# Kernel optimization log

Hardware: AMD Instinct MI355X
Metric: run time of the kernel (lower is better)

The kernel has to match this reference:

```python
import jax, jax.numpy as jnp
import numpy as np

EPS = 1e-12
TEMPERATURE = 0.1
QUEUE_SIZE = 1024
CUTOFF_KM = 25.0
EARTH_R_KM = 6371.0088


def _normalize(x, axis=-1):
    n = jnp.linalg.norm(x, axis=axis, keepdims=True)
    return x / jnp.maximum(n, EPS)


def _haversine_km(a, b):
    # a: (B,1,2), b: (1,S,2) in degrees (lat, lon) -> (B,S) km
    ra, rb = jnp.deg2rad(a), jnp.deg2rad(b)
    dlat = rb[..., 0] - ra[..., 0]
    dlon = rb[..., 1] - ra[..., 1]
    h = jnp.sin(dlat / 2) ** 2 + jnp.cos(ra[..., 0]) * jnp.cos(rb[..., 0]) * jnp.sin(dlon / 2) ** 2
    return 2.0 * EARTH_R_KM * jnp.arcsin(jnp.sqrt(jnp.clip(h, 0.0, 1.0)))


def setup_inputs() -> dict:
    key = jax.random.key(0)
    k1, k2, k3, k4, k5 = jax.random.split(key, 5)
    A, B, F, S = 3, 256, 512, 100000
    V = jax.random.normal(k1, (A, B, F), dtype=jnp.float32)
    L = jax.random.normal(k2, (B, F), dtype=jnp.float32)
    # gps as (lat, lon) degrees
    gps = jax.random.uniform(k3, (B, 2), dtype=jnp.float32) * jnp.array([120.0, 360.0]) - jnp.array([60.0, 180.0])
    support_feats = jax.random.normal(k4, (S, F), dtype=jnp.float32)
    support_gps = jax.random.uniform(k5, (S, 2), dtype=jnp.float32) * jnp.array([120.0, 360.0]) - jnp.array([60.0, 180.0])
    return {"V": V, "L": L, "gps": gps, "support_feats": support_feats, "support_gps": support_gps}


def reference(V, L, gps, support_feats, support_gps):
    T, Q = TEMPERATURE, QUEUE_SIZE
    L_norm = _normalize(L, axis=1)                      # (B,F)
    org = _normalize(V[0] * L_norm, axis=1)             # (B,F)
    aug = _normalize(V[1:] * L_norm, axis=2)            # (A-1,B,F)

    # nearest_neighbours (no_grad): per-batch NN in support set by dot-product sim
    sims = jnp.einsum('sf,bf->sb', support_feats, org)  # (S,B)
    nn_idx = jnp.argmax(sims, axis=0)                   # (B,)
    nn = _normalize(support_feats[nn_idx], axis=1)      # (B,F)
    nn = jax.lax.stop_gradient(nn)

    pos = jnp.exp(jnp.einsum('abf,bf->ab', aug, nn) / T)  # (A-1,B)
    batch_den = jnp.sum(pos, axis=0)                       # (B,)

    # nn_negative_queue (no_grad): first Q support rows farther than 25 km, zeros if fewer
    dist = _haversine_km(gps[:, None, :], support_gps[None, :, :])  # (B,S)
    far = dist > CUTOFF_KM                                          # (B,S)
    order = jnp.argsort(jnp.logical_not(far), axis=1)[:, :Q]        # stable: far rows first, in order
    valid = jnp.take_along_axis(far, order, axis=1)                 # (B,Q)
    negq = jnp.where(valid[..., None], support_feats[order], 0.0)   # (B,Q,F)
    negq = jax.lax.stop_gradient(_normalize(negq, axis=2))          # zero rows stay zero

    queue_den = jnp.sum(jnp.exp(jnp.einsum('bqf,bf->bq', negq, nn) / T), axis=1)  # (B,)

    loss = jnp.mean(-batch_den / (batch_den + queue_den))
    return loss
```

## Files before the change

kernel.cpp:

```cpp
#include <hip/hip_runtime.h>
#include <hip/hip_bf16.h>
#include <math.h>

#define B_N 256
#define F_N 512
#define S_N 100000
#define Q_N 1024
#define EPSF 1e-12f
#define BM 128
#define NBLK ((S_N + BM - 1) / BM)

typedef __attribute__((ext_vector_type(8))) short short8v;
typedef __attribute__((ext_vector_type(4))) float f32x4;

__device__ __forceinline__ unsigned short f2bf(float x) {
  unsigned u = __float_as_uint(x);
  u = u + 0x7FFFu + ((u >> 16) & 1u);
  return (unsigned short)(u >> 16);
}
__device__ __forceinline__ float bf2f(unsigned short h) {
  return __uint_as_float(((unsigned)h) << 16);
}

__device__ __forceinline__ float warpReduceSum(float v) {
  #pragma unroll
  for (int o = 32; o > 0; o >>= 1) v += __shfl_down(v, o);
  return v;
}

__device__ __forceinline__ float blockReduceSum256(float v, float* buf) {
  v = warpReduceSum(v);
  int lane = threadIdx.x & 63, w = threadIdx.x >> 6;
  __syncthreads();
  if (lane == 0) buf[w] = v;
  __syncthreads();
  return buf[0] + buf[1] + buf[2] + buf[3];
}

__device__ __forceinline__ void async_copy16(void* lds, const void* g) {
  __builtin_amdgcn_global_load_lds(
      (const __attribute__((address_space(1))) unsigned int*)g,
      (__attribute__((address_space(3))) unsigned int*)lds, 16, 0, 0);
}

__device__ __forceinline__ void cvt8(const float4 a, const float4 b,
                                     short8v& hi, short8v& lo) {
  union { unsigned u[4]; short8v v; } H, L;
  float xs[8] = {a.x, a.y, a.z, a.w, b.x, b.y, b.z, b.w};
  #pragma unroll
  for (int i = 0; i < 4; ++i) {
    float p = xs[2 * i], q = xs[2 * i + 1];
    union { __hip_bfloat162 b2; unsigned u; } c;
    c.b2 = __float22bfloat162_rn(make_float2(p, q));
    H.u[i] = c.u;
    float rp = p - __uint_as_float(c.u << 16);
    float rq = q - __uint_as_float(c.u & 0xFFFF0000u);
    union { __hip_bfloat162 b2; unsigned u; } d;
    d.b2 = __float22bfloat162_rn(make_float2(rp, rq));
    L.u[i] = d.u;
  }
  hi = H.v; lo = L.v;
}

__global__ __launch_bounds__(256) void k_prep(const float* __restrict__ V,
    const float* __restrict__ L, unsigned short* __restrict__ orgst,
    float* __restrict__ aug, unsigned long long* __restrict__ keys) {
  __shared__ float buf[4];
  int b = blockIdx.x, t = threadIdx.x;
  if (t == 0) keys[b] = 0ull;
  const float2 lv = *(const float2*)&L[b * F_N + t * 2];
  float ss = blockReduceSum256(lv.x * lv.x + lv.y * lv.y, buf);
  float invL = 1.0f / fmaxf(sqrtf(ss), EPSF);
  float lnx = lv.x * invL, lny = lv.y * invL;
  #pragma unroll
  for (int a = 0; a < 3; ++a) {
    const float2 vv = *(const float2*)&V[(a * B_N + b) * F_N + t * 2];
    float yx = vv.x * lnx, yy = vv.y * lny;
    float s2 = blockReduceSum256(yx * yx + yy * yy, buf);
    float inv = 1.0f / fmaxf(sqrtf(s2), EPSF);
    if (a == 0) {
      float ox = yx * inv, oy = yy * inv;
      int f = t * 2;
      int kt = f >> 5, kk = f & 31, sub = kk >> 3, pos = kk & 7;
      unsigned short hx = f2bf(ox), hy = f2bf(oy);
      unsigned short lx = f2bf(ox - bf2f(hx)), ly = f2bf(oy - bf2f(hy));
      int base = kt * 16384 + b * 64;
      ushort2 hv; hv.x = hx; hv.y = hy;
      ushort2 lw; lw.x = lx; lw.y = ly;
      *(ushort2*)&orgst[base + ((sub ^ (b & 7)) << 3) + pos] = hv;
      *(ushort2*)&orgst[base + (((sub | 4) ^ (b & 7)) << 3) + pos] = lw;
    } else {
      float* dst = &aug[((a - 1) * B_N + b) * F_N + t * 2];
      dst[0] = yx * inv;
      dst[1] = yy * inv;
    }
  }
}

__global__ __launch_bounds__(256, 3) void k_sims(const float* __restrict__ support,
    const unsigned short* __restrict__ orgst, unsigned long long* __restrict__ keys) {
  __shared__ __align__(16) unsigned char smem[32768];

  int t = threadIdx.x;
  int lane = t & 63, w = t >> 6;
  int r15 = lane & 15, ks = lane >> 4;
  int bid = blockIdx.x;
  int half = (bid >= NBLK) ? 1 : 0;
  int s0 = (half ? bid - NBLK : bid) * BM;

  f32x4 acc0[8], acc1[8];
  #pragma unroll
  for (int n = 0; n < 8; ++n) {
    acc0[n] = (f32x4){0.f, 0.f, 0.f, 0.f};
    acc1[n] = (f32x4){0.f, 0.f, 0.f, 0.f};
  }

  int row0 = s0 + w * 32 + r15;
  int row1 = row0 + 16;
  if (row0 > S_N - 1) row0 = S_N - 1;
  if (row1 > S_N - 1) row1 = S_N - 1;
  const float* ap0 = support + (size_t)row0 * F_N + ks * 8;
  const float* ap1 = support + (size_t)row1 * F_N + ks * 8;

  const unsigned char* bsrc =
      (const unsigned char*)orgst + half * 16384 + t * 16;

  {
    unsigned char* dst = smem + t * 16;
    #pragma unroll
    for (int p = 0; p < 4; ++p) async_copy16(dst + p * 4096, bsrc + p * 4096);
  }
  float4 a0a = *(const float4*)(ap0);
  float4 a0b = *(const float4*)(ap0 + 4);
  float4 a1a = *(const float4*)(ap1);
  float4 a1b = *(const float4*)(ap1 + 4);
  short8v fh0, fl0, fh1, fl1;
  cvt8(a0a, a0b, fh0, fl0);
  cvt8(a1a, a1b, fh1, fl1);
  __syncthreads();

  const int hioff = (ks ^ (r15 & 7)) << 4;
  const int looff = ((ks | 4) ^ (r15 & 7)) << 4;

  #pragma unroll 1
  for (int kt = 0; kt < 16; ++kt) {
    unsigned char* bbuf = smem + (kt & 1) * 16384;
    if (kt < 15) {
      a0a = *(const float4*)(ap0 + (kt + 1) * 32);
      a0b = *(const float4*)(ap0 + (kt + 1) * 32 + 4);
      a1a = *(const float4*)(ap1 + (kt + 1) * 32);
      a1b = *(const float4*)(ap1 + (kt + 1) * 32 + 4);
      __builtin_amdgcn_sched_barrier(0);
      const unsigned char* src = bsrc + (kt + 1) * 32768;
      unsigned char* dst = smem + ((kt + 1) & 1) * 16384 + t * 16;
      #pragma unroll
      for (int p = 0; p < 4; ++p) async_copy16(dst + p * 4096, src + p * 4096);
      __builtin_amdgcn_sched_barrier(0);
    }
    const unsigned char* bp = bbuf + r15 * 128 + hioff;
    const unsigned char* bq = bbuf + r15 * 128 + looff;
    __builtin_amdgcn_s_setprio(1);
    #pragma unroll
    for (int n = 0; n < 8; ++n) {
      short8v bh = *(const short8v*)(bp + n * 2048);
      short8v bl = *(const short8v*)(bq + n * 2048);
      acc0[n] = __builtin_amdgcn_mfma_f32_16x16x32_bf16(fh0, bh, acc0[n], 0, 0, 0);
      acc1[n] = __builtin_amdgcn_mfma_f32_16x16x32_bf16(fh1, bh, acc1[n], 0, 0, 0);
      acc0[n] = __builtin_amdgcn_mfma_f32_16x16x32_bf16(fl0, bh, acc0[n], 0, 0, 0);
      acc1[n] = __builtin_amdgcn_mfma_f32_16x16x32_bf16(fl1, bh, acc1[n], 0, 0, 0);
      acc0[n] = __builtin_amdgcn_mfma_f32_16x16x32_bf16(fh0, bl, acc0[n], 0, 0, 0);
      acc1[n] = __builtin_amdgcn_mfma_f32_16x16x32_bf16(fh1, bl, acc1[n], 0, 0, 0);
    }
    __builtin_amdgcn_s_setprio(0);
    __builtin_amdgcn_sched_barrier(0);
    if (kt < 15) {
      cvt8(a0a, a0b, fh0, fl0);
      cvt8(a1a, a1b, fh1, fl1);
      __builtin_amdgcn_sched_barrier(0);
      asm volatile("s_waitcnt vmcnt(0)" ::: "memory");
      __builtin_amdgcn_s_barrier();
      __builtin_amdgcn_sched_barrier(0);
    } else {
      __syncthreads();
    }
  }

  unsigned long long* wk = (unsigned long long*)smem;
  #pragma unroll
  for (int n = 0; n < 8; ++n) {
    float bv = -INFINITY;
    int bi = 0x7FFFFFFF;
    #pragma unroll
    for (int r = 0; r < 4; ++r) {
      int sA = s0 + w * 32 + ks * 4 + r;
      float vA = acc0[n][r];
      if (sA < S_N && (vA > bv || (vA == bv && sA < bi))) { bv = vA; bi = sA; }
      int sB = sA + 16;
      float vB = acc1[n][r];
      if (sB < S_N && (vB > bv || (vB == bv && sB < bi))) { bv = vB; bi = sB; }
    }
    #pragma unroll
    for (int mask = 16; mask <= 32; mask <<= 1) {
      float ov = __shfl_xor(bv, mask);
      int oi = __shfl_xor(bi, mask);
      if (ov > bv || (ov == bv && oi < bi)) { bv = ov; bi = oi; }
    }
    if (lane < 16) {
      unsigned u = __float_as_uint(bv);
      u = (u & 0x80000000u) ? ~u : (u | 0x80000000u);
      wk[w * 128 + n * 16 + lane] =
          ((unsigned long long)u << 32) |
          (unsigned long long)(0xFFFFFFFFu - (unsigned)bi);
    }
  }
  __syncthreads();
  if (t < 128) {
    unsigned long long k0 = wk[t], k1 = wk[128 + t];
    unsigned long long k2 = wk[256 + t], k3 = wk[384 + t];
    unsigned long long m01 = k0 > k1 ? k0 : k1;
    unsigned long long m23 = k2 > k3 ? k2 : k3;
    atomicMax(&keys[half * 128 + t], m01 > m23 ? m01 : m23);
  }
}

__global__ __launch_bounds__(256) void k_nn(const float* __restrict__ support,
    const unsigned long long* __restrict__ keys, const float* __restrict__ aug,
    float* __restrict__ nn, float* __restrict__ bden) {
  __shared__ float buf[4];
  int b = blockIdx.x, t = threadIdx.x;
  int idx = (int)(0xFFFFFFFFu - (unsigned)(keys[b] & 0xFFFFFFFFull));
  const float2 rv = *(const float2*)&support[(size_t)idx * F_N + t * 2];
  float ss = blockReduceSum256(rv.x * rv.x + rv.y * rv.y, buf);
  float inv = 1.0f / fmaxf(sqrtf(ss), EPSF);
  float nx = rv.x * inv, ny = rv.y * inv;
  nn[b * F_N + t * 2] = nx;
  nn[b * F_N + t * 2 + 1] = ny;
  const float2 a0 = *(const float2*)&aug[(0 * B_N + b) * F_N + t * 2];
  const float2 a1 = *(const float2*)&aug[(1 * B_N + b) * F_N + t * 2];
  float d0 = blockReduceSum256(a0.x * nx + a0.y * ny, buf);
  float d1 = blockReduceSum256(a1.x * nx + a1.y * ny, buf);
  if (t == 0) bden[b] = expf(d0 * 10.0f) + expf(d1 * 10.0f);
}

__global__ __launch_bounds__(256) void k_qdot(const float* __restrict__ support,
    const float* __restrict__ gps, const float* __restrict__ sgps,
    const float* __restrict__ nn, double* __restrict__ qpart) {
  __shared__ float nns[F_N];
  __shared__ int qi[256];
  __shared__ int wtot[4];
  __shared__ double wacc[4];
  int b = blockIdx.x >> 2, c = blockIdx.x & 3;
  int t = threadIdx.x;
  int lane = t & 63, w = t >> 6;

  *(float2*)&nns[t * 2] = *(const float2*)&nn[b * F_N + t * 2];

  const float DEG2RAD = 0.017453292519943295f;
  float la = gps[b * 2] * DEG2RAD;
  float lo = gps[b * 2 + 1] * DEG2RAD;
  float ca = cosf(la);
  double xd = 25.0 / (2.0 * 6371.0088);
  float hcut = (float)(sin(xd) * sin(xd));

  int cnt = 0;
  int qlo = c * 256;
  for (int base = 0; base < S_N; base += 256) {
    int s = base + t;
    bool far = false;
    if (s < S_N) {
      float lb = sgps[s * 2] * DEG2RAD;
      float ob = sgps[s * 2 + 1] * DEG2RAD;
      float sl = sinf((lb - la) * 0.5f);
      float so = sinf((ob - lo) * 0.5f);
      float h = sl * sl + ca * cosf(lb) * so * so;
      far = h > hcut;
    }
    unsigned long long m = __ballot(far);
    if (lane == 0) wtot[w] = (int)__popcll(m);
    __syncthreads();
    int offs = cnt;
    for (int wi = 0; wi < w; ++wi) offs += wtot[wi];
    if (far) {
      int pos = offs + (int)__popcll(m & ((1ull << lane) - 1ull));
      int rel = pos - qlo;
      if (rel >= 0 && rel < 256) qi[rel] = s;
    }
    cnt += wtot[0] + wtot[1] + wtot[2] + wtot[3];
    __syncthreads();
    if (cnt >= Q_N) break;
  }
  int nvalid = cnt < Q_N ? cnt : Q_N;
  __syncthreads();

  double acc = 0.0;
  for (int j = 0; j < 64; ++j) {
    int q = qlo + w * 64 + j;
    if (q >= nvalid) break;
    int row = qi[w * 64 + j];
    const float4* rp = (const float4*)&support[(size_t)row * F_N + lane * 8];
    float4 r0 = rp[0], r1 = rp[1];
    const float4 n0 = *(const float4*)&nns[lane * 8];
    const float4 n1 = *(const float4*)&nns[lane * 8 + 4];
    float dot = r0.x * n0.x + r0.y * n0.y + r0.z * n0.z + r0.w * n0.w +
                r1.x * n1.x + r1.y * n1.y + r1.z * n1.z + r1.w * n1.w;
    float ssq = r0.x * r0.x + r0.y * r0.y + r0.z * r0.z + r0.w * r0.w +
                r1.x * r1.x + r1.y * r1.y + r1.z * r1.z + r1.w * r1.w;
    #pragma unroll
    for (int o = 32; o > 0; o >>= 1) {
      dot += __shfl_xor(dot, o);
      ssq += __shfl_xor(ssq, o);
    }
    float val = dot / fmaxf(sqrtf(ssq), EPSF);
    acc += (double)expf(val * 10.0f);
  }
  if (lane == 0) wacc[w] = acc;
  __syncthreads();
  if (t == 0) {
    int got = nvalid - qlo;
    if (got < 0) got = 0; if (got > 256) got = 256;
    int inval = 256 - got;
    qpart[blockIdx.x] = wacc[0] + wacc[1] + wacc[2] + wacc[3] + (double)inval;
  }
}

__global__ __launch_bounds__(256) void k_final(const double* __restrict__ qpart,
    const float* __restrict__ bden, float* __restrict__ out) {
  __shared__ double buf[4];
  int t = threadIdx.x;
  double qd = qpart[t * 4] + qpart[t * 4 + 1] + qpart[t * 4 + 2] + qpart[t * 4 + 3];
  double bd = (double)bden[t];
  double v = -bd / (bd + qd);
  #pragma unroll
  for (int o = 32; o > 0; o >>= 1) v += __shfl_down(v, o);
  if ((t & 63) == 0) buf[t >> 6] = v;
  __syncthreads();
  if (t == 0) out[0] = (float)((buf[0] + buf[1] + buf[2] + buf[3]) / 256.0);
}

extern "C" void kernel_launch(void* const* d_in, const int* in_sizes, int n_in,
                              void* d_out, int out_size, void* d_ws, size_t ws_size,
                              hipStream_t stream) {
  const float* V = (const float*)d_in[0];
  const float* L = (const float*)d_in[1];
  const float* gps = (const float*)d_in[2];
  const float* support = (const float*)d_in[3];
  const float* sgps = (const float*)d_in[4];
  float* out = (float*)d_out;

  char* ws = (char*)d_ws;
  unsigned long long* keys = (unsigned long long*)ws;
  float* bden = (float*)(ws + 2048);
  double* qpart = (double*)(ws + 4096);
  unsigned short* orgst = (unsigned short*)(ws + 12288);
  float* aug = (float*)(ws + 12288 + 524288);
  float* nn = (float*)(ws + 12288 + 524288 + 1048576);

  k_prep<<<256, 256, 0, stream>>>(V, L, orgst, aug, keys);
  k_sims<<<2 * NBLK, 256, 0, stream>>>(support, orgst, keys);
  k_nn<<<256, 256, 0, stream>>>(support, keys, aug, nn, bden);
  k_qdot<<<1024, 256, 0, stream>>>(support, gps, sgps, nn, qpart);
  k_final<<<1, 256, 0, stream>>>(qpart, bden, out);
}
```

Before: 190.6 us.

## Use single-bf16 sims with per-block maxima, then exact FP64 rescoring of candidates

Result: no change. 191.8 us (+0.6%).

```diff
diff --git a/kernel.cpp b/kernel.cpp
--- a/kernel.cpp
+++ b/kernel.cpp
@@ -9,6 +9,8 @@
 #define EPSF 1e-12f
 #define BM 128
 #define NBLK ((S_N + BM - 1) / BM)
+#define CAND_MAX 64
+#define MARGIN 0.125f
 
 typedef __attribute__((ext_vector_type(8))) short short8v;
 typedef __attribute__((ext_vector_type(4))) float f32x4;
@@ -18,9 +20,6 @@
   u = u + 0x7FFFu + ((u >> 16) & 1u);
   return (unsigned short)(u >> 16);
 }
-__device__ __forceinline__ float bf2f(unsigned short h) {
-  return __uint_as_float(((unsigned)h) << 16);
-}
 
 __device__ __forceinline__ float warpReduceSum(float v) {
   #pragma unroll
@@ -43,31 +42,22 @@
       (__attribute__((address_space(3))) unsigned int*)lds, 16, 0, 0);
 }
 
-__device__ __forceinline__ void cvt8(const float4 a, const float4 b,
-                                     short8v& hi, short8v& lo) {
-  union { unsigned u[4]; short8v v; } H, L;
-  float xs[8] = {a.x, a.y, a.z, a.w, b.x, b.y, b.z, b.w};
-  #pragma unroll
-  for (int i = 0; i < 4; ++i) {
-    float p = xs[2 * i], q = xs[2 * i + 1];
-    union { __hip_bfloat162 b2; unsigned u; } c;
-    c.b2 = __float22bfloat162_rn(make_float2(p, q));
-    H.u[i] = c.u;
-    float rp = p - __uint_as_float(c.u << 16);
-    float rq = q - __uint_as_float(c.u & 0xFFFF0000u);
-    union { __hip_bfloat162 b2; unsigned u; } d;
-    d.b2 = __float22bfloat162_rn(make_float2(rp, rq));
-    L.u[i] = d.u;
-  }
-  hi = H.v; lo = L.v;
+__device__ __forceinline__ void cvt8hi(const float4 a, const float4 b,
+                                       short8v& hi) {
+  union { unsigned u[4]; short8v v; } H;
+  union { __hip_bfloat162 b2; unsigned u; } c;
+  c.b2 = __float22bfloat162_rn(make_float2(a.x, a.y)); H.u[0] = c.u;
+  c.b2 = __float22bfloat162_rn(make_float2(a.z, a.w)); H.u[1] = c.u;
+  c.b2 = __float22bfloat162_rn(make_float2(b.x, b.y)); H.u[2] = c.u;
+  c.b2 = __float22bfloat162_rn(make_float2(b.z, b.w)); H.u[3] = c.u;
+  hi = H.v;
 }
 
 __global__ __launch_bounds__(256) void k_prep(const float* __restrict__ V,
-    const float* __restrict__ L, unsigned short* __restrict__ orgst,
-    float* __restrict__ aug, unsigned long long* __restrict__ keys) {
+    const float* __restrict__ L, unsigned short* __restrict__ orghi,
+    float* __restrict__ org, float* __restrict__ aug) {
   __shared__ float buf[4];
   int b = blockIdx.x, t = threadIdx.x;
-  if (t == 0) keys[b] = 0ull;
   const float2 lv = *(const float2*)&L[b * F_N + t * 2];
   float ss = blockReduceSum256(lv.x * lv.x + lv.y * lv.y, buf);
   float invL = 1.0f / fmaxf(sqrtf(ss), EPSF);
@@ -82,13 +72,11 @@
       float ox = yx * inv, oy = yy * inv;
       int f = t * 2;
       int kt = f >> 5, kk = f & 31, sub = kk >> 3, pos = kk & 7;
-      unsigned short hx = f2bf(ox), hy = f2bf(oy);
-      unsigned short lx = f2bf(ox - bf2f(hx)), ly = f2bf(oy - bf2f(hy));
-      int base = kt * 16384 + b * 64;
-      ushort2 hv; hv.x = hx; hv.y = hy;
-      ushort2 lw; lw.x = lx; lw.y = ly;
-      *(ushort2*)&orgst[base + ((sub ^ (b & 7)) << 3) + pos] = hv;
-      *(ushort2*)&orgst[base + (((sub | 4) ^ (b & 7)) << 3) + pos] = lw;
+      int off = kt * 8192 + b * 32 + ((sub ^ ((b >> 1) & 3)) << 3) + pos;
+      ushort2 hv; hv.x = f2bf(ox); hv.y = f2bf(oy);
+      *(ushort2*)&orghi[off] = hv;
+      float2 of; of.x = ox; of.y = oy;
+      *(float2*)&org[b * F_N + f] = of;
     } else {
       float* dst = &aug[((a - 1) * B_N + b) * F_N + t * 2];
       dst[0] = yx * inv;
@@ -97,20 +85,18 @@
   }
 }
 
-__global__ __launch_bounds__(256, 3) void k_sims(const float* __restrict__ support,
-    const unsigned short* __restrict__ orgst, unsigned long long* __restrict__ keys) {
+__global__ __launch_bounds__(256, 2) void k_sims(const float* __restrict__ support,
+    const unsigned short* __restrict__ orghi, float* __restrict__ blkmax) {
   __shared__ __align__(16) unsigned char smem[32768];
 
   int t = threadIdx.x;
   int lane = t & 63, w = t >> 6;
   int r15 = lane & 15, ks = lane >> 4;
-  int bid = blockIdx.x;
-  int half = (bid >= NBLK) ? 1 : 0;
-  int s0 = (half ? bid - NBLK : bid) * BM;
-
-  f32x4 acc0[8], acc1[8];
-  #pragma unroll
-  for (int n = 0; n < 8; ++n) {
+  int s0 = blockIdx.x * BM;
+
+  f32x4 acc0[16], acc1[16];
+  #pragma unroll
+  for (int n = 0; n < 16; ++n) {
     acc0[n] = (f32x4){0.f, 0.f, 0.f, 0.f};
     acc1[n] = (f32x4){0.f, 0.f, 0.f, 0.f};
   }
@@ -122,113 +108,159 @@
   const float* ap0 = support + (size_t)row0 * F_N + ks * 8;
   const float* ap1 = support + (size_t)row1 * F_N + ks * 8;
 
-  const unsigned char* bsrc =
-      (const unsigned char*)orgst + half * 16384 + t * 16;
+  const unsigned char* bsrc = (const unsigned char*)orghi + t * 16;
 
   {
     unsigned char* dst = smem + t * 16;
     #pragma unroll
     for (int p = 0; p < 4; ++p) async_copy16(dst + p * 4096, bsrc + p * 4096);
   }
+  __builtin_amdgcn_sched_barrier(0);
   float4 a0a = *(const float4*)(ap0);
   float4 a0b = *(const float4*)(ap0 + 4);
   float4 a1a = *(const float4*)(ap1);
   float4 a1b = *(const float4*)(ap1 + 4);
-  short8v fh0, fl0, fh1, fl1;
-  cvt8(a0a, a0b, fh0, fl0);
-  cvt8(a1a, a1b, fh1, fl1);
-  __syncthreads();
-
-  const int hioff = (ks ^ (r15 & 7)) << 4;
-  const int looff = ((ks | 4) ^ (r15 & 7)) << 4;
+  __builtin_amdgcn_sched_barrier(0);
+  __syncthreads();
+
+  const int rbase = r15 * 64 + ((ks ^ ((r15 >> 1) & 3)) << 4);
 
   #pragma unroll 1
   for (int kt = 0; kt < 16; ++kt) {
     unsigned char* bbuf = smem + (kt & 1) * 16384;
+    short8v fh0, fh1;
+    cvt8hi(a0a, a0b, fh0);
+    cvt8hi(a1a, a1b, fh1);
     if (kt < 15) {
+      const unsigned char* src = bsrc + (kt + 1) * 16384;
+      unsigned char* dst = smem + ((kt + 1) & 1) * 16384 + t * 16;
+      #pragma unroll
+      for (int p = 0; p < 4; ++p) async_copy16(dst + p * 4096, src + p * 4096);
+      __builtin_amdgcn_sched_barrier(0);
       a0a = *(const float4*)(ap0 + (kt + 1) * 32);
       a0b = *(const float4*)(ap0 + (kt + 1) * 32 + 4);
       a1a = *(const float4*)(ap1 + (kt + 1) * 32);
       a1b = *(const float4*)(ap1 + (kt + 1) * 32 + 4);
       __builtin_amdgcn_sched_barrier(0);
-      const unsigned char* src = bsrc + (kt + 1) * 32768;
-      unsigned char* dst = smem + ((kt + 1) & 1) * 16384 + t * 16;
-      #pragma unroll
-      for (int p = 0; p < 4; ++p) async_copy16(dst + p * 4096, src + p * 4096);
-      __builtin_amdgcn_sched_barrier(0);
-    }
-    const unsigned char* bp = bbuf + r15 * 128 + hioff;
-    const unsigned char* bq = bbuf + r15 * 128 + looff;
+    }
+    const unsigned char* bp = bbuf + rbase;
     __builtin_amdgcn_s_setprio(1);
     #pragma unroll
-    for (int n = 0; n < 8; ++n) {
-      short8v bh = *(const short8v*)(bp + n * 2048);
-      short8v bl = *(const short8v*)(bq + n * 2048);
+    for (int n = 0; n < 16; ++n) {
+      short8v bh = *(const short8v*)(bp + n * 1024);
       acc0[n] = __builtin_amdgcn_mfma_f32_16x16x32_bf16(fh0, bh, acc0[n], 0, 0, 0);
       acc1[n] = __builtin_amdgcn_mfma_f32_16x16x32_bf16(fh1, bh, acc1[n], 0, 0, 0);
-      acc0[n] = __builtin_amdgcn_mfma_f32_16x16x32_bf16(fl0, bh, acc0[n], 0, 0, 0);
-      acc1[n] = __builtin_amdgcn_mfma_f32_16x16x32_bf16(fl1, bh, acc1[n], 0, 0, 0);
-      acc0[n] = __builtin_amdgcn_mfma_f32_16x16x32_bf16(fh0, bl, acc0[n], 0, 0, 0);
-      acc1[n] = __builtin_amdgcn_mfma_f32_16x16x32_bf16(fh1, bl, acc1[n], 0, 0, 0);
     }
     __builtin_amdgcn_s_setprio(0);
     __builtin_amdgcn_sched_barrier(0);
     if (kt < 15) {
-      cvt8(a0a, a0b, fh0, fl0);
-      cvt8(a1a, a1b, fh1, fl1);
-      __builtin_amdgcn_sched_barrier(0);
-      asm volatile("s_waitcnt vmcnt(0)" ::: "memory");
+      asm volatile("s_waitcnt vmcnt(4)" ::: "memory");
       __builtin_amdgcn_s_barrier();
-      __builtin_amdgcn_sched_barrier(0);
     } else {
       __syncthreads();
     }
-  }
-
-  unsigned long long* wk = (unsigned long long*)smem;
-  #pragma unroll
-  for (int n = 0; n < 8; ++n) {
+    __builtin_amdgcn_sched_barrier(0);
+  }
+
+  float* wkf = (float*)smem;
+  #pragma unroll
+  for (int n = 0; n < 16; ++n) {
     float bv = -INFINITY;
-    int bi = 0x7FFFFFFF;
     #pragma unroll
     for (int r = 0; r < 4; ++r) {
-      int sA = s0 + w * 32 + ks * 4 + r;
-      float vA = acc0[n][r];
-      if (sA < S_N && (vA > bv || (vA == bv && sA < bi))) { bv = vA; bi = sA; }
-      int sB = sA + 16;
-      float vB = acc1[n][r];
-      if (sB < S_N && (vB > bv || (vB == bv && sB < bi))) { bv = vB; bi = sB; }
-    }
-    #pragma unroll
-    for (int mask = 16; mask <= 32; mask <<= 1) {
-      float ov = __shfl_xor(bv, mask);
-      int oi = __shfl_xor(bi, mask);
-      if (ov > bv || (ov == bv && oi < bi)) { bv = ov; bi = oi; }
-    }
-    if (lane < 16) {
-      unsigned u = __float_as_uint(bv);
-      u = (u & 0x80000000u) ? ~u : (u | 0x80000000u);
-      wk[w * 128 + n * 16 + lane] =
-          ((unsigned long long)u << 32) |
-          (unsigned long long)(0xFFFFFFFFu - (unsigned)bi);
-    }
-  }
-  __syncthreads();
-  if (t < 128) {
-    unsigned long long k0 = wk[t], k1 = wk[128 + t];
-    unsigned long long k2 = wk[256 + t], k3 = wk[384 + t];
-    unsigned long long m01 = k0 > k1 ? k0 : k1;
-    unsigned long long m23 = k2 > k3 ? k2 : k3;
-    atomicMax(&keys[half * 128 + t], m01 > m23 ? m01 : m23);
+      bv = fmaxf(bv, acc0[n][r]);
+      bv = fmaxf(bv, acc1[n][r]);
+    }
+    bv = fmaxf(bv, __shfl_xor(bv, 16));
+    bv = fmaxf(bv, __shfl_xor(bv, 32));
+    if (lane < 16) wkf[w * 256 + n * 16 + lane] = bv;
+  }
+  __syncthreads();
+  {
+    float m4 = fmaxf(fmaxf(wkf[t], wkf[256 + t]),
+                     fmaxf(wkf[512 + t], wkf[768 + t]));
+    blkmax[(size_t)t * NBLK + blockIdx.x] = m4;
+  }
+}
+
+__global__ __launch_bounds__(256) void k_picknn(const float* __restrict__ support,
+    const float* __restrict__ org, const float* __restrict__ blkmax,
+    int* __restrict__ nnidx) {
+  __shared__ float orgs[F_N];
+  __shared__ float redf[4];
+  __shared__ int lcand[CAND_MAX];
+  __shared__ int lcnt;
+  __shared__ double rv[4];
+  __shared__ int ri[4];
+  int b = blockIdx.x, t = threadIdx.x;
+  int lane = t & 63, w = t >> 6;
+
+  orgs[t] = org[b * F_N + t];
+  orgs[256 + t] = org[b * F_N + 256 + t];
+  if (t == 0) lcnt = 0;
+
+  const float* bm = blkmax + (size_t)b * NBLK;
+  float mx = -INFINITY;
+  for (int rb = t; rb < NBLK; rb += 256) mx = fmaxf(mx, bm[rb]);
+  #pragma unroll
+  for (int o = 32; o > 0; o >>= 1) mx = fmaxf(mx, __shfl_xor(mx, o));
+  __syncthreads();
+  if (lane == 0) redf[w] = mx;
+  __syncthreads();
+  mx = fmaxf(fmaxf(redf[0], redf[1]), fmaxf(redf[2], redf[3]));
+  float thr = mx - MARGIN;
+
+  for (int rb = t; rb < NBLK; rb += 256) {
+    if (bm[rb] >= thr) {
+      int sl = atomicAdd(&lcnt, 1);
+      if (sl < CAND_MAX) lcand[sl] = rb;
+    }
+  }
+  __syncthreads();
+  int nc = lcnt < CAND_MAX ? lcnt : CAND_MAX;
+
+  double bv = -1e300;
+  int bi = 0x7FFFFFFF;
+  for (int task = t; task < nc * BM; task += 256) {
+    int c = task >> 7, r = task & (BM - 1);
+    int s = lcand[c] * BM + r;
+    if (s < S_N) {
+      const float* rp = support + (size_t)s * F_N;
+      double d0 = 0, d1 = 0, d2 = 0, d3 = 0;
+      #pragma unroll 4
+      for (int k = 0; k < F_N; k += 4) {
+        d0 += (double)rp[k] * (double)orgs[k];
+        d1 += (double)rp[k + 1] * (double)orgs[k + 1];
+        d2 += (double)rp[k + 2] * (double)orgs[k + 2];
+        d3 += (double)rp[k + 3] * (double)orgs[k + 3];
+      }
+      double dv = (d0 + d1) + (d2 + d3);
+      if (dv > bv || (dv == bv && s < bi)) { bv = dv; bi = s; }
+    }
+  }
+  #pragma unroll
+  for (int o = 32; o > 0; o >>= 1) {
+    double ov = __shfl_xor(bv, o);
+    int oi = __shfl_xor(bi, o);
+    if (ov > bv || (ov == bv && oi < bi)) { bv = ov; bi = oi; }
+  }
+  if (lane == 0) { rv[w] = bv; ri[w] = bi; }
+  __syncthreads();
+  if (t == 0) {
+    double fv = rv[0]; int fi = ri[0];
+    #pragma unroll
+    for (int i = 1; i < 4; ++i)
+      if (rv[i] > fv || (rv[i] == fv && ri[i] < fi)) { fv = rv[i]; fi = ri[i]; }
+    nnidx[b] = fi;
   }
 }
 
 __global__ __launch_bounds__(256) void k_nn(const float* __restrict__ support,
-    const unsigned long long* __restrict__ keys, const float* __restrict__ aug,
+    const int* __restrict__ nnidx, const float* __restrict__ aug,
     float* __restrict__ nn, float* __restrict__ bden) {
   __shared__ float buf[4];
   int b = blockIdx.x, t = threadIdx.x;
-  int idx = (int)(0xFFFFFFFFu - (unsigned)(keys[b] & 0xFFFFFFFFull));
+  int idx = nnidx[b];
   const float2 rv = *(const float2*)&support[(size_t)idx * F_N + t * 2];
   float ss = blockReduceSum256(rv.x * rv.x + rv.y * rv.y, buf);
   float inv = 1.0f / fmaxf(sqrtf(ss), EPSF);
@@ -348,16 +380,19 @@
   float* out = (float*)d_out;
 
   char* ws = (char*)d_ws;
-  unsigned long long* keys = (unsigned long long*)ws;
+  int* nnidx = (int*)ws;
   float* bden = (float*)(ws + 2048);
   double* qpart = (double*)(ws + 4096);
-  unsigned short* orgst = (unsigned short*)(ws + 12288);
-  float* aug = (float*)(ws + 12288 + 524288);
-  float* nn = (float*)(ws + 12288 + 524288 + 1048576);
-
-  k_prep<<<256, 256, 0, stream>>>(V, L, orgst, aug, keys);
-  k_sims<<<2 * NBLK, 256, 0, stream>>>(support, orgst, keys);
-  k_nn<<<256, 256, 0, stream>>>(support, keys, aug, nn, bden);
+  unsigned short* orghi = (unsigned short*)(ws + 12288);
+  float* org = (float*)(ws + 12288 + 262144);
+  float* aug = (float*)(ws + 12288 + 262144 + 524288);
+  float* nn = (float*)(ws + 12288 + 262144 + 524288 + 1048576);
+  float* blkmax = (float*)(ws + 12288 + 262144 + 524288 + 1048576 + 524288);
+
+  k_prep<<<256, 256, 0, stream>>>(V, L, orghi, org, aug);
+  k_sims<<<NBLK, 256, 0, stream>>>(support, orghi, blkmax);
+  k_picknn<<<256, 256, 0, stream>>>(support, org, blkmax, nnidx);
+  k_nn<<<256, 256, 0, stream>>>(support, nnidx, aug, nn, bden);
   k_qdot<<<1024, 256, 0, stream>>>(support, gps, sgps, nn, qpart);
   k_final<<<1, 256, 0, stream>>>(qpart, bden, out);
 }
```
